# Optimization experiments

Hardware: AMD Instinct MI355X
Metric: run time of the kernel (lower is better)

The kernel has to match this reference:

```python
import jax, jax.numpy as jnp
import numpy as np

DIM = 2048
NUM_HEADS = 8
HEAD_DIM = DIM // NUM_HEADS
BATCH = 16384
EPS = 1e-5


def setup_inputs() -> dict:
    key = jax.random.key(0)
    ks = jax.random.split(key, 10)
    s = 1.0 / np.sqrt(DIM)
    inp = {
        "x": jax.random.normal(ks[0], (BATCH, 1, DIM), dtype=jnp.float32),
        "w_q": jax.random.uniform(ks[1], (DIM, DIM), jnp.float32, -s, s),
        "b_q": jax.random.uniform(ks[2], (DIM,), jnp.float32, -s, s),
        "w_k": jax.random.uniform(ks[3], (DIM, DIM), jnp.float32, -s, s),
        "b_k": jax.random.uniform(ks[4], (DIM,), jnp.float32, -s, s),
        "w_v": jax.random.uniform(ks[5], (DIM, DIM), jnp.float32, -s, s),
        "b_v": jax.random.uniform(ks[6], (DIM,), jnp.float32, -s, s),
        "w_o": jax.random.uniform(ks[7], (DIM, DIM), jnp.float32, -s, s),
        "b_o": jax.random.uniform(ks[8], (DIM,), jnp.float32, -s, s),
        "ln_gamma": jnp.ones((DIM,), jnp.float32),
        "ln_beta": jnp.zeros((DIM,), jnp.float32),
    }
    return inp


def _layer_norm(x, gamma, beta):
    mean = jnp.mean(x, axis=-1, keepdims=True)
    var = jnp.mean(jnp.square(x - mean), axis=-1, keepdims=True)
    return (x - mean) * jax.lax.rsqrt(var + EPS) * gamma + beta


def reference(x, w_q, b_q, w_k, b_k, w_v, b_v, w_o, b_o, ln_gamma, ln_beta):
    # x: (B, 1, D). Dropout is identity (eval mode).
    residual = x
    h = _layer_norm(x, ln_gamma, ln_beta)
    q = h @ w_q.T + b_q  # (B, 1, D)
    k = h @ w_k.T + b_k
    v = h @ w_v.T + b_v
    B = x.shape[0]
    # (B, H, 1, hd)
    qh = q.reshape(B, 1, NUM_HEADS, HEAD_DIM).transpose(0, 2, 1, 3)
    kh = k.reshape(B, 1, NUM_HEADS, HEAD_DIM).transpose(0, 2, 1, 3)
    vh = v.reshape(B, 1, NUM_HEADS, HEAD_DIM).transpose(0, 2, 1, 3)
    scale = HEAD_DIM ** -0.5
    # (B, H, 1, 1); with seq_len=1 softmax is trivially 1, but keep the math faithful
    scores = jnp.einsum("bhqd,bhkd->bhqk", qh, kh) * scale
    probs = jax.nn.softmax(scores, axis=-1)
    attn = jnp.einsum("bhqk,bhkd->bhqd", probs, vh)  # (B, H, 1, hd)
    attn = attn.transpose(0, 2, 1, 3).reshape(B, 1, DIM)
    out = attn @ w_o.T + b_o
    out = out + residual
    return out[:, 0, :]  # squeeze seq dim -> (B, D)
```

## Files before the change

kernel.cpp:

```cpp
#include <hip/hip_runtime.h>
#include <hip/hip_bf16.h>
#include <cstdint>

#define D_MODEL 2048
#define N_BATCH 16384

typedef __attribute__((ext_vector_type(8))) __bf16 bf16x8;
typedef __attribute__((ext_vector_type(4))) float f32x4;

__device__ __forceinline__ unsigned short f2bf(float f) {
    unsigned int u = __builtin_bit_cast(unsigned int, f);
    u += 0x7fffu + ((u >> 16) & 1u);
    return (unsigned short)(u >> 16);
}

__global__ __launch_bounds__(256) void prep_kernel(
    const float* __restrict__ w_v, const float* __restrict__ w_o,
    const float* __restrict__ b_v, const float* __restrict__ b_o,
    unsigned short* __restrict__ wvT, unsigned short* __restrict__ woB,
    float* __restrict__ b_c)
{
    __shared__ float tile[32][33];
    const int b = blockIdx.x;
    const int t = threadIdx.x;
    if (b < 4096) {
        const int nb = 64;
        const int k0 = (b % nb) * 32;
        const int j0 = (b / nb) * 32;
        const int tx = t & 31, ty0 = t >> 5;
        #pragma unroll
        for (int i = 0; i < 32; i += 8) {
            int j = ty0 + i;
            tile[j][tx] = w_v[(long)(j0 + j) * D_MODEL + k0 + tx];
        }
        __syncthreads();
        #pragma unroll
        for (int i = 0; i < 32; i += 8) {
            int kk = ty0 + i;
            wvT[(long)(k0 + kk) * D_MODEL + j0 + tx] = f2bf(tile[tx][kk]);
        }
    } else if (b < 6144) {
        long i = ((long)(b - 4096) * 256 + t) * 8;
        const float4* in4 = reinterpret_cast<const float4*>(w_o + i);
        float4 a = in4[0], bb = in4[1];
        union { unsigned short u[8]; uint4 v; } o;
        o.u[0] = f2bf(a.x); o.u[1] = f2bf(a.y); o.u[2] = f2bf(a.z); o.u[3] = f2bf(a.w);
        o.u[4] = f2bf(bb.x); o.u[5] = f2bf(bb.y); o.u[6] = f2bf(bb.z); o.u[7] = f2bf(bb.w);
        *reinterpret_cast<uint4*>(woB + i) = o.v;
    } else {
        const int n = b - 6144;
        const float4* w4 = reinterpret_cast<const float4*>(w_o + (long)n * D_MODEL);
        const float4* v4 = reinterpret_cast<const float4*>(b_v);
        float4 a = w4[t], bb = w4[256 + t], va = v4[t], vb = v4[256 + t];
        float s = a.x*va.x + a.y*va.y + a.z*va.z + a.w*va.w
                + bb.x*vb.x + bb.y*vb.y + bb.z*vb.z + bb.w*vb.w;
        #pragma unroll
        for (int off = 32; off; off >>= 1) s += __shfl_xor(s, off);
        float* red = &tile[0][0];
        const int lane = t & 63, wid = t >> 6;
        if (lane == 0) red[wid] = s;
        __syncthreads();
        if (t == 0) b_c[n] = red[0] + red[1] + red[2] + red[3] + b_o[n];
    }
}

__global__ __launch_bounds__(256) void lnwc_kernel(
    const unsigned short* __restrict__ A, const unsigned short* __restrict__ B,
    unsigned short* __restrict__ C,
    const float* __restrict__ x, const float* __restrict__ gamma,
    const float* __restrict__ beta, unsigned short* __restrict__ h)
{
    __shared__ __align__(16) unsigned short Alds[128 * 32];
    __shared__ __align__(16) unsigned short Blds[128 * 32];
    const int t = threadIdx.x;

    if (blockIdx.x < 256) {
        const int K = D_MODEL, N = D_MODEL;
        int wg = blockIdx.x;
        wg = (wg & 7) * 32 + (wg >> 3);
        const int bm = wg >> 4, bn = wg & 15;

        const int lane = t & 63, wid = t >> 6;
        const int wr = wid >> 1, wc = wid & 1;

        f32x4 acc[4][4];
        #pragma unroll
        for (int i = 0; i < 4; i++)
            #pragma unroll
            for (int j = 0; j < 4; j++) acc[i][j] = (f32x4){0.f, 0.f, 0.f, 0.f};

        const long Abase = (long)bm * 128 * K;
        const long Bbase = (long)bn * 128 * K;
        const int ci0 = wid * 64 + lane;
        const int ci1 = 256 + ci0;
        const int r0 = ci0 >> 2, c0 = (ci0 & 3) * 8;
        const int r1 = ci1 >> 2, c1 = (ci1 & 3) * 8;

        const int arow = wr * 64 + (lane & 15);
        const int brow = wc * 64 + (lane & 15);
        const int koff = (lane >> 4) * 8;

        for (int k0 = 0; k0 < K; k0 += 32) {
            __builtin_amdgcn_global_load_lds(
                (const __attribute__((address_space(1))) void*)(A + Abase + (long)r0 * K + k0 + c0),
                (__attribute__((address_space(3))) void*)(Alds + wid * 512), 16, 0, 0);
            __builtin_amdgcn_global_load_lds(
                (const __attribute__((address_space(1))) void*)(A + Abase + (long)r1 * K + k0 + c1),
                (__attribute__((address_space(3))) void*)(Alds + 2048 + wid * 512), 16, 0, 0);
            __builtin_amdgcn_global_load_lds(
                (const __attribute__((address_space(1))) void*)(B + Bbase + (long)r0 * K + k0 + c0),
                (__attribute__((address_space(3))) void*)(Blds + wid * 512), 16, 0, 0);
            __builtin_amdgcn_global_load_lds(
                (const __attribute__((address_space(1))) void*)(B + Bbase + (long)r1 * K + k0 + c1),
                (__attribute__((address_space(3))) void*)(Blds + 2048 + wid * 512), 16, 0, 0);
            __syncthreads();

            bf16x8 af[4], bfr[4];
            #pragma unroll
            for (int m = 0; m < 4; m++)
                af[m] = *reinterpret_cast<const bf16x8*>(&Alds[(arow + m * 16) * 32 + koff]);
            #pragma unroll
            for (int n = 0; n < 4; n++)
                bfr[n] = *reinterpret_cast<const bf16x8*>(&Blds[(brow + n * 16) * 32 + koff]);
            #pragma unroll
            for (int m = 0; m < 4; m++)
                #pragma unroll
                for (int n = 0; n < 4; n++)
                    acc[m][n] = __builtin_amdgcn_mfma_f32_16x16x32_bf16(af[m], bfr[n], acc[m][n], 0, 0, 0);
            __syncthreads();
        }

        const int crow0 = bm * 128 + wr * 64 + ((lane >> 4) << 2);
        const int ccol0 = bn * 128 + wc * 64 + (lane & 15);
        #pragma unroll
        for (int m = 0; m < 4; m++)
            #pragma unroll
            for (int j = 0; j < 4; j++) {
                const long r = crow0 + m * 16 + j;
                #pragma unroll
                for (int n = 0; n < 4; n++)
                    C[r * N + ccol0 + n * 16] = f2bf(acc[m][n][j]);
            }
    } else {
        const int row = blockIdx.x - 256;
        const float4* x4 = reinterpret_cast<const float4*>(x + (long)row * D_MODEL);
        float4 a = x4[t];
        float4 b = x4[256 + t];
        float s  = a.x + a.y + a.z + a.w + b.x + b.y + b.z + b.w;
        float ss = a.x*a.x + a.y*a.y + a.z*a.z + a.w*a.w
                 + b.x*b.x + b.y*b.y + b.z*b.z + b.w*b.w;
        #pragma unroll
        for (int off = 32; off; off >>= 1) {
            s  += __shfl_xor(s, off);
            ss += __shfl_xor(ss, off);
        }
        float* red = reinterpret_cast<float*>(Alds);
        const int lane = t & 63, wid = t >> 6;
        if (lane == 0) { red[wid*2] = s; red[wid*2+1] = ss; }
        __syncthreads();
        s  = red[0] + red[2] + red[4] + red[6];
        ss = red[1] + red[3] + red[5] + red[7];
        const float mean = s * (1.0f / D_MODEL);
        const float var  = ss * (1.0f / D_MODEL) - mean * mean;
        const float inv  = rsqrtf(var + 1e-5f);

        const float4* g4  = reinterpret_cast<const float4*>(gamma);
        const float4* be4 = reinterpret_cast<const float4*>(beta);
        ushort4* h4 = reinterpret_cast<ushort4*>(h + (long)row * D_MODEL);
        {
            float4 g = g4[t], be = be4[t];
            ushort4 o;
            o.x = f2bf((a.x - mean) * inv * g.x + be.x);
            o.y = f2bf((a.y - mean) * inv * g.y + be.y);
            o.z = f2bf((a.z - mean) * inv * g.z + be.z);
            o.w = f2bf((a.w - mean) * inv * g.w + be.w);
            h4[t] = o;
        }
        {
            float4 g = g4[256 + t], be = be4[256 + t];
            ushort4 o;
            o.x = f2bf((b.x - mean) * inv * g.x + be.x);
            o.y = f2bf((b.y - mean) * inv * g.y + be.y);
            o.z = f2bf((b.z - mean) * inv * g.z + be.z);
            o.w = f2bf((b.w - mean) * inv * g.w + be.w);
            h4[256 + t] = o;
        }
    }
}

#define GLL(src, dst) __builtin_amdgcn_global_load_lds( \
    (const __attribute__((address_space(1))) void*)(src), \
    (__attribute__((address_space(3))) void*)(dst), 16, 0, 0)
#define WAITV4() do { asm volatile("s_waitcnt vmcnt(4)" ::: "memory"); \
                      __builtin_amdgcn_sched_barrier(0); } while (0)
#define WAITV0() do { asm volatile("s_waitcnt vmcnt(0)" ::: "memory"); \
                      __builtin_amdgcn_sched_barrier(0); } while (0)

__global__ __launch_bounds__(512, 2) void gemm_bt_8ph(
    const unsigned short* __restrict__ A, const unsigned short* __restrict__ B,
    float* __restrict__ C, const float* __restrict__ bias,
    const float* __restrict__ resid, int M, int N, int K)
{
    __shared__ __align__(16) char ldsb[131072];

    const int nBN = N >> 8;
    int wg = blockIdx.x;
    const int cpx = gridDim.x >> 3;
    wg = (wg & 7) * cpx + (wg >> 3);
    const int bm = wg / nBN, bn = wg % nBN;

    const int t = threadIdx.x;
    const int lane = t & 63, wid = t >> 6;
    const int wr = wid >> 2;
    const int wc = wid & 3;

    const long Kl = K;
    const int tr = t >> 3;
    const int c8 = ((t & 7) ^ (tr & 7)) * 8;
    const unsigned short* As = A + (long)(bm * 256 + tr) * Kl + c8;
    const unsigned short* Bs = B + (long)(bn * 256 + tr) * Kl + c8;

#define ST_A(buf, half, kcol) do { \
    const unsigned short* s_ = As + (half) * 128 * Kl + (kcol); \
    char* d_ = ldsb + (buf) * 65536 + (half) * 16384 + t * 16; \
    GLL(s_, d_); GLL(s_ + 64 * Kl, d_ + 8192); } while (0)
#define ST_B(buf, half, kcol) do { \
    const unsigned short* s_ = Bs + (half) * 128 * Kl + (kcol); \
    char* d_ = ldsb + (buf) * 65536 + 32768 + (half) * 16384 + t * 16; \
    GLL(s_, d_); GLL(s_ + 64 * Kl, d_ + 8192); } while (0)

    const int l15 = lane & 15, l4 = lane >> 4;
    const int swz0 = ((l4)     ^ (l15 & 7)) << 4;
    const int swz1 = ((4 + l4) ^ (l15 & 7)) << 4;
    const int aOff = wr * 16384 + l15 * 128;
    const int bOff = 32768 + (wc >> 1) * 16384 + ((wc & 1) * 64 + l15) * 128;

#define LDV(off) (*reinterpret_cast<const bf16x8*>(ldsb + (off)))
#define RD_A(buf, mh) do { _Pragma("unroll") for (int mi = 0; mi < 4; ++mi) { \
    af[mi][0] = LDV((buf) * 65536 + aOff + ((mh) * 4 + mi) * 2048 + swz0); \
    af[mi][1] = LDV((buf) * 65536 + aOff + ((mh) * 4 + mi) * 2048 + swz1); } } while (0)
#define RD_B0(buf) do { _Pragma("unroll") for (int nj = 0; nj < 2; ++nj) { \
    b0[nj][0] = LDV((buf) * 65536 + bOff + nj * 2048 + swz0); \
    b0[nj][1] = LDV((buf) * 65536 + bOff + nj * 2048 + swz1); } } while (0)
#define RD_B1(buf) do { _Pragma("unroll") for (int nj = 0; nj < 2; ++nj) { \
    b1[nj][0] = LDV((buf) * 65536 + bOff + (2 + nj) * 2048 + swz0); \
    b1[nj][1] = LDV((buf) * 65536 + bOff + (2 + nj) * 2048 + swz1); } } while (0)

#define MMQ(mh, nh, BQ) do { \
    __builtin_amdgcn_s_barrier(); \
    asm volatile("s_waitcnt lgkmcnt(0)" ::: "memory"); \
    __builtin_amdgcn_sched_barrier(0); \
    __builtin_amdgcn_s_setprio(1); \
    _Pragma("unroll") for (int kk = 0; kk < 2; ++kk) \
    _Pragma("unroll") for (int mi = 0; mi < 4; ++mi) \
    _Pragma("unroll") for (int nj = 0; nj < 2; ++nj) \
        acc[(mh) * 4 + mi][(nh) * 2 + nj] = __builtin_amdgcn_mfma_f32_16x16x32_bf16( \
            af[mi][kk], BQ[nj][kk], acc[(mh) * 4 + mi][(nh) * 2 + nj], 0, 0, 0); \
    __builtin_amdgcn_s_setprio(0); } while (0)
#define ENDP() __builtin_amdgcn_s_barrier()

    bf16x8 af[4][2], b0[2][2], b1[2][2];
    f32x4 acc[8][4];
    #pragma unroll
    for (int i = 0; i < 8; i++)
        #pragma unroll
        for (int j = 0; j < 4; j++) acc[i][j] = (f32x4){0.f, 0.f, 0.f, 0.f};

    const int NI = K >> 7;

    ST_A(0, 0, 0); ST_A(0, 1, 0); ST_B(0, 0, 0); ST_B(0, 1, 0);
    ST_B(1, 0, 64); ST_A(1, 0, 64);
    WAITV4();
    __builtin_amdgcn_s_barrier();

    for (int i = 0; i < NI; ++i) {
        const int kcA1 = (i << 7) + 64;
        const int kcN0 = (i << 7) + 128;
        const int kcN1 = (i << 7) + 192;
        const bool more = (i + 1 < NI);

        RD_A(0, 0); RD_B0(0);
        ST_A(1, 1, kcA1);
        MMQ(0, 0, b0); ENDP();
        RD_B1(0);
        ST_B(1, 1, kcA1);
        MMQ(0, 1, b1); ENDP();
        RD_A(0, 1);
        if (more) ST_B(0, 0, kcN0);
        MMQ(1, 0, b0); ENDP();
        if (more) ST_A(0, 0, kcN0);
        MMQ(1, 1, b1);
        if (more) { WAITV4(); } else { WAITV0(); }
        ENDP();
        RD_A(1, 0); RD_B0(1);
        if (more) ST_A(0, 1, kcN0);
        MMQ(0, 0, b0); ENDP();
        RD_B1(1);
        if (more) ST_B(0, 1, kcN0);
        MMQ(0, 1, b1); ENDP();
        RD_A(1, 1);
        if (more) ST_B(1, 0, kcN1);
        MMQ(1, 0, b0); ENDP();
        if (more) ST_A(1, 0, kcN1);
        MMQ(1, 1, b1);
        if (more) { WAITV4(); }
        ENDP();
    }
#undef ST_A
#undef ST_B
#undef RD_A
#undef RD_B0
#undef RD_B1
#undef MMQ
#undef ENDP
#undef LDV

    const int crow0 = bm * 256 + wr * 128 + l4 * 4;
    const int ccol0 = bn * 256 + wc * 64 + l15;
    #pragma unroll
    for (int m = 0; m < 8; m++)
        #pragma unroll
        for (int j = 0; j < 4; j++) {
            const long r = crow0 + m * 16 + j;
            float* crow = C + r * N;
            const float* rrow = resid + r * N;
            #pragma unroll
            for (int n = 0; n < 4; n++) {
                const int col = ccol0 + n * 16;
                crow[col] = acc[m][n][j] + bias[col] + rrow[col];
            }
        }
}

extern "C" void kernel_launch(void* const* d_in, const int* in_sizes, int n_in,
                              void* d_out, int out_size, void* d_ws, size_t ws_size,
                              hipStream_t stream) {
    const float* x     = (const float*)d_in[0];
    const float* w_v   = (const float*)d_in[5];
    const float* b_v   = (const float*)d_in[6];
    const float* w_o   = (const float*)d_in[7];
    const float* b_o   = (const float*)d_in[8];
    const float* gamma = (const float*)d_in[9];
    const float* beta  = (const float*)d_in[10];
    float* out = (float*)d_out;

    char* ws = (char*)d_ws;
    unsigned short* h   = (unsigned short*)(ws);
    unsigned short* wvT = (unsigned short*)(ws + 67108864L);
    unsigned short* woB = (unsigned short*)(ws + 67108864L + 8388608L);
    unsigned short* Wc  = (unsigned short*)(ws + 67108864L + 2 * 8388608L);
    float*          b_c = (float*)(ws + 67108864L + 3 * 8388608L);

    prep_kernel<<<8192, 256, 0, stream>>>(w_v, w_o, b_v, b_o, wvT, woB, b_c);
    lnwc_kernel<<<256 + N_BATCH, 256, 0, stream>>>(woB, wvT, Wc, x, gamma, beta, h);
    gemm_bt_8ph<<<(N_BATCH / 256) * (D_MODEL / 256), 512, 0, stream>>>(
        h, Wc, out, b_c, x, N_BATCH, D_MODEL, D_MODEL);
}
```

Measured before the change: 232.7 us.

## Replace 256x256 eight-phase GEMM with simpler 128x128 double-buffered kernel

Swaps the 256x256-tile, 512-thread GEMM and its interleaved eight-phase load/MFMA schedule for a 128x128-tile, 256-thread kernel. The new kernel uses a plain double buffer with 64-wide K steps and one barrier pair per step. Bias values are hoisted into registers for the epilogue. The smaller tile uses less LDS and fewer registers per block, allowing more resident blocks, but it halves operand reuse per tile and drops the fine-grained overlap of loads with compute.

Measured after the change: 240.2 us. +3.2%, slower.

```diff
diff --git a/kernel.cpp b/kernel.cpp
--- a/kernel.cpp
+++ b/kernel.cpp
@@ -191,19 +191,15 @@
 #define GLL(src, dst) __builtin_amdgcn_global_load_lds( \
     (const __attribute__((address_space(1))) void*)(src), \
     (__attribute__((address_space(3))) void*)(dst), 16, 0, 0)
-#define WAITV4() do { asm volatile("s_waitcnt vmcnt(4)" ::: "memory"); \
-                      __builtin_amdgcn_sched_barrier(0); } while (0)
-#define WAITV0() do { asm volatile("s_waitcnt vmcnt(0)" ::: "memory"); \
-                      __builtin_amdgcn_sched_barrier(0); } while (0)
-
-__global__ __launch_bounds__(512, 2) void gemm_bt_8ph(
+
+__global__ __launch_bounds__(256, 2) void gemm_bt_128r(
     const unsigned short* __restrict__ A, const unsigned short* __restrict__ B,
     float* __restrict__ C, const float* __restrict__ bias,
     const float* __restrict__ resid, int M, int N, int K)
 {
-    __shared__ __align__(16) char ldsb[131072];
-
-    const int nBN = N >> 8;
+    __shared__ __align__(16) char ldsb[65536];
+
+    const int nBN = N >> 7;
     int wg = blockIdx.x;
     const int cpx = gridDim.x >> 3;
     wg = (wg & 7) * cpx + (wg >> 3);
@@ -211,114 +207,84 @@
 
     const int t = threadIdx.x;
     const int lane = t & 63, wid = t >> 6;
-    const int wr = wid >> 2;
-    const int wc = wid & 3;
+    const int wr = wid >> 1, wc = wid & 1;
 
     const long Kl = K;
     const int tr = t >> 3;
-    const int c8 = ((t & 7) ^ (tr & 7)) * 8;
-    const unsigned short* As = A + (long)(bm * 256 + tr) * Kl + c8;
-    const unsigned short* Bs = B + (long)(bn * 256 + tr) * Kl + c8;
-
-#define ST_A(buf, half, kcol) do { \
-    const unsigned short* s_ = As + (half) * 128 * Kl + (kcol); \
-    char* d_ = ldsb + (buf) * 65536 + (half) * 16384 + t * 16; \
-    GLL(s_, d_); GLL(s_ + 64 * Kl, d_ + 8192); } while (0)
-#define ST_B(buf, half, kcol) do { \
-    const unsigned short* s_ = Bs + (half) * 128 * Kl + (kcol); \
-    char* d_ = ldsb + (buf) * 65536 + 32768 + (half) * 16384 + t * 16; \
-    GLL(s_, d_); GLL(s_ + 64 * Kl, d_ + 8192); } while (0)
+    const int chA = ((t & 7) ^ (tr & 7)) * 8;
+    const unsigned short* As = A + (long)(bm * 128 + tr) * Kl + chA;
+    const unsigned short* Bs = B + (long)(bn * 128 + tr) * Kl + chA;
+
+#define STAGE(buf, kcol) do { \
+    char* da_ = ldsb + (buf) * 32768 + t * 16; \
+    char* db_ = da_ + 16384; \
+    _Pragma("unroll") for (int rnd = 0; rnd < 4; ++rnd) \
+        GLL(As + (long)(rnd * 32) * Kl + (kcol), da_ + rnd * 4096); \
+    _Pragma("unroll") for (int rnd = 0; rnd < 4; ++rnd) \
+        GLL(Bs + (long)(rnd * 32) * Kl + (kcol), db_ + rnd * 4096); } while (0)
 
     const int l15 = lane & 15, l4 = lane >> 4;
-    const int swz0 = ((l4)     ^ (l15 & 7)) << 4;
-    const int swz1 = ((4 + l4) ^ (l15 & 7)) << 4;
-    const int aOff = wr * 16384 + l15 * 128;
-    const int bOff = 32768 + (wc >> 1) * 16384 + ((wc & 1) * 64 + l15) * 128;
+    const int swz0 = (((0 + l4) ^ (l15 & 7)) << 4);
+    const int swz1 = (((4 + l4) ^ (l15 & 7)) << 4);
+    const int aRow = (wr * 64 + l15) * 128;
+    const int bRow = 16384 + (wc * 64 + l15) * 128;
 
 #define LDV(off) (*reinterpret_cast<const bf16x8*>(ldsb + (off)))
-#define RD_A(buf, mh) do { _Pragma("unroll") for (int mi = 0; mi < 4; ++mi) { \
-    af[mi][0] = LDV((buf) * 65536 + aOff + ((mh) * 4 + mi) * 2048 + swz0); \
-    af[mi][1] = LDV((buf) * 65536 + aOff + ((mh) * 4 + mi) * 2048 + swz1); } } while (0)
-#define RD_B0(buf) do { _Pragma("unroll") for (int nj = 0; nj < 2; ++nj) { \
-    b0[nj][0] = LDV((buf) * 65536 + bOff + nj * 2048 + swz0); \
-    b0[nj][1] = LDV((buf) * 65536 + bOff + nj * 2048 + swz1); } } while (0)
-#define RD_B1(buf) do { _Pragma("unroll") for (int nj = 0; nj < 2; ++nj) { \
-    b1[nj][0] = LDV((buf) * 65536 + bOff + (2 + nj) * 2048 + swz0); \
-    b1[nj][1] = LDV((buf) * 65536 + bOff + (2 + nj) * 2048 + swz1); } } while (0)
-
-#define MMQ(mh, nh, BQ) do { \
-    __builtin_amdgcn_s_barrier(); \
-    asm volatile("s_waitcnt lgkmcnt(0)" ::: "memory"); \
-    __builtin_amdgcn_sched_barrier(0); \
-    __builtin_amdgcn_s_setprio(1); \
-    _Pragma("unroll") for (int kk = 0; kk < 2; ++kk) \
-    _Pragma("unroll") for (int mi = 0; mi < 4; ++mi) \
-    _Pragma("unroll") for (int nj = 0; nj < 2; ++nj) \
-        acc[(mh) * 4 + mi][(nh) * 2 + nj] = __builtin_amdgcn_mfma_f32_16x16x32_bf16( \
-            af[mi][kk], BQ[nj][kk], acc[(mh) * 4 + mi][(nh) * 2 + nj], 0, 0, 0); \
-    __builtin_amdgcn_s_setprio(0); } while (0)
-#define ENDP() __builtin_amdgcn_s_barrier()
-
-    bf16x8 af[4][2], b0[2][2], b1[2][2];
-    f32x4 acc[8][4];
+
+    f32x4 acc[4][4];
     #pragma unroll
-    for (int i = 0; i < 8; i++)
+    for (int i = 0; i < 4; i++)
         #pragma unroll
         for (int j = 0; j < 4; j++) acc[i][j] = (f32x4){0.f, 0.f, 0.f, 0.f};
 
-    const int NI = K >> 7;
-
-    ST_A(0, 0, 0); ST_A(0, 1, 0); ST_B(0, 0, 0); ST_B(0, 1, 0);
-    ST_B(1, 0, 64); ST_A(1, 0, 64);
-    WAITV4();
-    __builtin_amdgcn_s_barrier();
-
-    for (int i = 0; i < NI; ++i) {
-        const int kcA1 = (i << 7) + 64;
-        const int kcN0 = (i << 7) + 128;
-        const int kcN1 = (i << 7) + 192;
-        const bool more = (i + 1 < NI);
-
-        RD_A(0, 0); RD_B0(0);
-        ST_A(1, 1, kcA1);
-        MMQ(0, 0, b0); ENDP();
-        RD_B1(0);
-        ST_B(1, 1, kcA1);
-        MMQ(0, 1, b1); ENDP();
-        RD_A(0, 1);
-        if (more) ST_B(0, 0, kcN0);
-        MMQ(1, 0, b0); ENDP();
-        if (more) ST_A(0, 0, kcN0);
-        MMQ(1, 1, b1);
-        if (more) { WAITV4(); } else { WAITV0(); }
-        ENDP();
-        RD_A(1, 0); RD_B0(1);
-        if (more) ST_A(0, 1, kcN0);
-        MMQ(0, 0, b0); ENDP();
-        RD_B1(1);
-        if (more) ST_B(0, 1, kcN0);
-        MMQ(0, 1, b1); ENDP();
-        RD_A(1, 1);
-        if (more) ST_B(1, 0, kcN1);
-        MMQ(1, 0, b0); ENDP();
-        if (more) ST_A(1, 0, kcN1);
-        MMQ(1, 1, b1);
-        if (more) { WAITV4(); }
-        ENDP();
+    const int nt = K >> 6;
+    STAGE(0, 0);
+
+    int buf = 0;
+    for (int kt = 0; kt < nt; ++kt) {
+        if (kt + 1 < nt) {
+            STAGE(buf ^ 1, (kt + 1) << 6);
+            asm volatile("s_waitcnt vmcnt(8)" ::: "memory");
+        } else {
+            asm volatile("s_waitcnt vmcnt(0)" ::: "memory");
+        }
+        __builtin_amdgcn_sched_barrier(0);
+        __builtin_amdgcn_s_barrier();
+
+        const int bb = buf * 32768;
+        bf16x8 af[4][2], bfr[4][2];
+        #pragma unroll
+        for (int mi = 0; mi < 4; ++mi) {
+            af[mi][0] = LDV(bb + aRow + mi * 2048 + swz0);
+            af[mi][1] = LDV(bb + aRow + mi * 2048 + swz1);
+        }
+        #pragma unroll
+        for (int nj = 0; nj < 4; ++nj) {
+            bfr[nj][0] = LDV(bb + bRow + nj * 2048 + swz0);
+            bfr[nj][1] = LDV(bb + bRow + nj * 2048 + swz1);
+        }
+        #pragma unroll
+        for (int kk = 0; kk < 2; ++kk)
+            #pragma unroll
+            for (int mi = 0; mi < 4; ++mi)
+                #pragma unroll
+                for (int nj = 0; nj < 4; ++nj)
+                    acc[mi][nj] = __builtin_amdgcn_mfma_f32_16x16x32_bf16(
+                        af[mi][kk], bfr[nj][kk], acc[mi][nj], 0, 0, 0);
+
+        __builtin_amdgcn_s_barrier();
+        buf ^= 1;
     }
-#undef ST_A
-#undef ST_B
-#undef RD_A
-#undef RD_B0
-#undef RD_B1
-#undef MMQ
-#undef ENDP
+#undef STAGE
 #undef LDV
 
-    const int crow0 = bm * 256 + wr * 128 + l4 * 4;
-    const int ccol0 = bn * 256 + wc * 64 + l15;
+    const int crow0 = bm * 128 + wr * 64 + l4 * 4;
+    const int ccol0 = bn * 128 + wc * 64 + l15;
+    float bias4[4];
     #pragma unroll
-    for (int m = 0; m < 8; m++)
+    for (int n = 0; n < 4; n++) bias4[n] = bias[ccol0 + n * 16];
+    #pragma unroll
+    for (int m = 0; m < 4; m++)
         #pragma unroll
         for (int j = 0; j < 4; j++) {
             const long r = crow0 + m * 16 + j;
@@ -327,7 +293,7 @@
             #pragma unroll
             for (int n = 0; n < 4; n++) {
                 const int col = ccol0 + n * 16;
-                crow[col] = acc[m][n][j] + bias[col] + rrow[col];
+                crow[col] = acc[m][n][j] + bias4[n] + rrow[col];
             }
         }
 }
@@ -353,6 +319,6 @@
 
     prep_kernel<<<8192, 256, 0, stream>>>(w_v, w_o, b_v, b_o, wvT, woB, b_c);
     lnwc_kernel<<<256 + N_BATCH, 256, 0, stream>>>(woB, wvT, Wc, x, gamma, beta, h);
-    gemm_bt_8ph<<<(N_BATCH / 256) * (D_MODEL / 256), 512, 0, stream>>>(
+    gemm_bt_128r<<<(N_BATCH / 128) * (D_MODEL / 128), 256, 0, stream>>>(
         h, Wc, out, b_c, x, N_BATCH, D_MODEL, D_MODEL);
 }
```
